# Kernel tuning notes

Measured on AMD Instinct MI355X. Metric: run time of the kernel, lower is better.

## Reference

```python
import jax, jax.numpy as jnp
import numpy as np

# Static config (matches init_kwargs)
H, G, D = 16, 4, 128          # n_head, n_query_groups, head_size
QPK = H // G                  # queries per kv group = 4
LEFT = 1024 - 1               # sliding-window left width (local_window-1)
SCALE = 1.0 / float(np.sqrt(D))
NEG = jnp.finfo(jnp.float32).min


def _rope(x, cos, sin):
    # x: [B,T,h,D]; cos/sin: [T, D/2]; non-interleaved (flash-attn) convention
    d2 = cos.shape[-1]
    x1, x2 = x[..., :d2], x[..., d2:]
    c = cos[None, :, None, :]
    s = sin[None, :, None, :]
    return jnp.concatenate([x1 * c - x2 * s, x1 * s + x2 * c], axis=-1)


def setup_inputs() -> dict:
    key = jax.random.key(0)
    ks = jax.random.split(key, 4)
    B, T, C = 1, 2048, 2048
    x = jax.random.normal(ks[0], (B, T, C), jnp.float32)
    # real RoPE tables, base 10000
    pos = jnp.arange(T, dtype=jnp.float32)
    inv_freq = 1.0 / (10000.0 ** (jnp.arange(0, D, 2, dtype=jnp.float32) / D))
    ang = pos[:, None] * inv_freq[None, :]        # [T, D/2]
    cos, sin = jnp.cos(ang), jnp.sin(ang)
    W_attn = jax.random.normal(ks[1], ((H + 2 * G) * D, C), jnp.float32) * 0.02
    W_proj = jax.random.normal(ks[2], (C, H * D), jnp.float32) * 0.02
    k_sink = jax.random.normal(ks[3], (G * D,), jnp.float32) * 0.02
    v_sink = jnp.zeros((G * D,), jnp.float32)     # buffer, zeros in original
    return {"x": x, "cos": cos, "sin": sin, "W_attn": W_attn,
            "W_proj": W_proj, "k_sink": k_sink, "v_sink": v_sink}


def reference(x, cos, sin, W_attn, W_proj, k_sink, v_sink):
    B, T, C = x.shape
    # fused QKV projection (no bias)
    qkv = jnp.einsum('btc,oc->bto', x, W_attn)                 # [B,T,(H+2G)*D]
    qkv = qkv.reshape(B, T, G, QPK + 2, D)
    q = qkv[:, :, :, :QPK, :].reshape(B, T, H, D)              # [B,T,H,D]
    k = qkv[:, :, :, QPK, :]                                   # [B,T,G,D]
    v = qkv[:, :, :, QPK + 1, :]                               # [B,T,G,D]
    # RoPE on q and k
    q = _rope(q, cos, sin)
    k = _rope(k, cos, sin)
    # prepend sink token to k/v -> seqlen_k = T+1
    k = jnp.concatenate([jnp.broadcast_to(k_sink.reshape(1, 1, G, D), (B, 1, G, D)), k], axis=1)
    v = jnp.concatenate([jnp.broadcast_to(v_sink.reshape(1, 1, G, D), (B, 1, G, D)), v], axis=1)
    Tk = T + 1
    # GQA: group-major query head layout -> head h uses kv group h // QPK
    kh = jnp.repeat(k, QPK, axis=2)                            # [B,Tk,H,D]
    vh = jnp.repeat(v, QPK, axis=2)
    scores = jnp.einsum('bqhd,bkhd->bhqk', q, kh) * SCALE      # [B,H,T,Tk]
    # flash-attn causal + sliding window, bottom-right aligned: offset = Tk - T
    off = Tk - T
    i = jnp.arange(T)[:, None]
    j = jnp.arange(Tk)[None, :]
    allowed = (j <= i + off) & (j >= i + off - LEFT)
    scores = jnp.where(allowed[None, None], scores, NEG)
    p = jax.nn.softmax(scores, axis=-1)
    o = jnp.einsum('bhqk,bkhd->bqhd', p, vh).reshape(B, T, H * D)
    y = jnp.einsum('btd,cd->btc', o, W_proj)                   # output proj, no bias
    return y
```

## Files before the change

### kernel.cpp

```cpp
#include <hip/hip_runtime.h>

#define T_SEQ  2048
#define TK_SEQ 2049
#define JP     2080
#define SL_F    0.12751744f
#define THR_L2  11.0f

typedef __attribute__((ext_vector_type(8))) short short8;
typedef __attribute__((ext_vector_type(4))) float f32x4;

__device__ __forceinline__ unsigned short f2bf(float f) {
  unsigned int u = __float_as_uint(f);
  u += 0x7fff + ((u >> 16) & 1);
  return (unsigned short)(u >> 16);
}

__device__ __forceinline__ void gload16(const unsigned short* g, unsigned short* l) {
  __builtin_amdgcn_global_load_lds(
      (const __attribute__((address_space(1))) void*)g,
      (__attribute__((address_space(3))) void*)l, 16, 0, 0);
}

__global__ __launch_bounds__(256) void split_pack(const float4* __restrict__ s0,
                                                  unsigned short* __restrict__ d0,
                                                  int n0, int p0,
                                                  const float4* __restrict__ s1,
                                                  unsigned short* __restrict__ d1,
                                                  int n1, int p1) {
  int i = blockIdx.x * 256 + threadIdx.x;
  const float4* s; unsigned short* d; int k, p;
  if (i < n0) { s = s0; d = d0; k = i; p = p0; }
  else { k = i - n0; if (k >= n1) return; s = s1; d = d1; p = p1; }
  float4 f = s[k];
  float fv[4] = {f.x, f.y, f.z, f.w};
  ushort4 hv, lv;
#pragma unroll
  for (int e = 0; e < 4; ++e) {
    unsigned int u = __float_as_uint(fv[e]) & 0xffff0000u;
    ((unsigned short*)&hv)[e] = (unsigned short)(u >> 16);
    ((unsigned short*)&lv)[e] = f2bf(fv[e] - __uint_as_float(u));
  }
  *(ushort4*)(d + 4 * (size_t)k)     = hv;
  *(ushort4*)(d + p + 4 * (size_t)k) = lv;
}

__global__ __launch_bounds__(256, 3) void gemm_sp(const unsigned short* __restrict__ Ag,
                                                  const unsigned short* __restrict__ Bg,
                                                  float* __restrict__ C,
                                                  int M, int N, int K) {
  __shared__ unsigned short Ah[128 * 32], Al[128 * 32];
  __shared__ unsigned short Bh[64 * 32],  Bl[64 * 32];

  const int tid  = threadIdx.x;
  const int lane = tid & 63;
  const int wid  = tid >> 6;
  const int wm   = (wid >> 1) << 6;
  const int wn   = (wid & 1) << 5;
  const int lo16 = lane & 15;
  const int hi4  = lane >> 4;
  const int m0   = blockIdx.y << 7;
  const int n0   = blockIdx.x << 6;
  const size_t MK = (size_t)M * K;
  const size_t NK = (size_t)N * K;

  const int ca0 = (wid << 6) + lane;
  const int ca1 = ((4 + wid) << 6) + lane;
  const int cb  = (wid << 6) + lane;
  const unsigned short* a0g = Ag + (size_t)(m0 + (ca0 >> 2)) * K + ((ca0 & 3) << 3);
  const unsigned short* a1g = Ag + (size_t)(m0 + (ca1 >> 2)) * K + ((ca1 & 3) << 3);
  const unsigned short* bg  = Bg + (size_t)(n0 + (cb  >> 2)) * K + ((cb  & 3) << 3);
  unsigned short* a0d  = &Ah[wid << 9];
  unsigned short* a1d  = &Ah[(4 + wid) << 9];
  unsigned short* al0d = &Al[wid << 9];
  unsigned short* al1d = &Al[(4 + wid) << 9];
  unsigned short* bhd  = &Bh[wid << 9];
  unsigned short* bld  = &Bl[wid << 9];

  int ra[4], rb[2];
#pragma unroll
  for (int i = 0; i < 4; ++i) ra[i] = ((wm + i * 16 + lo16) << 5) + (hi4 << 3);
#pragma unroll
  for (int j = 0; j < 2; ++j) rb[j] = ((wn + j * 16 + lo16) << 5) + (hi4 << 3);

  f32x4 acc[4][2];
  const f32x4 z4 = {0.f, 0.f, 0.f, 0.f};
#pragma unroll
  for (int i = 0; i < 4; ++i)
#pragma unroll
    for (int j = 0; j < 2; ++j) acc[i][j] = z4;

  for (int k0 = 0; k0 < K; k0 += 32) {
    __syncthreads();
    gload16(a0g + k0, a0d);
    gload16(a1g + k0, a1d);
    gload16(a0g + MK + k0, al0d);
    gload16(a1g + MK + k0, al1d);
    gload16(bg + k0, bhd);
    gload16(bg + NK + k0, bld);
    __syncthreads();

    short8 fah[4], fal[4], fbh[2], fbl[2];
#pragma unroll
    for (int i = 0; i < 4; ++i) {
      fah[i] = *(const short8*)&Ah[ra[i]];
      fal[i] = *(const short8*)&Al[ra[i]];
    }
#pragma unroll
    for (int j = 0; j < 2; ++j) {
      fbh[j] = *(const short8*)&Bh[rb[j]];
      fbl[j] = *(const short8*)&Bl[rb[j]];
    }
#pragma unroll
    for (int i = 0; i < 4; ++i)
#pragma unroll
      for (int j = 0; j < 2; ++j) {
        acc[i][j] = __builtin_amdgcn_mfma_f32_16x16x32_bf16(fah[i], fbh[j], acc[i][j], 0, 0, 0);
        acc[i][j] = __builtin_amdgcn_mfma_f32_16x16x32_bf16(fal[i], fbh[j], acc[i][j], 0, 0, 0);
        acc[i][j] = __builtin_amdgcn_mfma_f32_16x16x32_bf16(fah[i], fbl[j], acc[i][j], 0, 0, 0);
      }
  }

#pragma unroll
  for (int i = 0; i < 4; ++i) {
    const int row = m0 + wm + i * 16 + (hi4 << 2);
#pragma unroll
    for (int j = 0; j < 2; ++j) {
      float* cp = C + (size_t)row * N + n0 + wn + j * 16 + lo16;
      cp[0]            = acc[i][j][0];
      cp[(size_t)N]    = acc[i][j][1];
      cp[(size_t)2*N]  = acc[i][j][2];
      cp[(size_t)3*N]  = acc[i][j][3];
    }
  }
}

#define RB_Q  4096
#define RB_K  1024
#define RB_KE 64
#define RB_V  65

__global__ __launch_bounds__(256) void rope2(const float* __restrict__ qkv,
                                             const float* __restrict__ cosb,
                                             const float* __restrict__ sinb,
                                             const float* __restrict__ ksink,
                                             const float* __restrict__ vsink,
                                             unsigned short* __restrict__ qb,
                                             unsigned short* __restrict__ kb,
                                             unsigned short* __restrict__ vtb) {
  __shared__ unsigned short tl[512 * 33];
  const int bid = blockIdx.x, tid = threadIdx.x;
  if (bid < RB_Q) {
    int idx = bid * 256 + tid;
    int t = idx >> 9, rem = idx & 511;
    int h = rem >> 5, dp = (rem & 31) << 1;
    int g = h >> 2, qi = h & 3;
    const float* src = qkv + (size_t)t * 3072 + g * 768 + qi * 128;
    float2 x1 = *(const float2*)(src + dp);
    float2 x2 = *(const float2*)(src + 64 + dp);
    float2 c  = *(const float2*)(cosb + t * 64 + dp);
    float2 s  = *(const float2*)(sinb + t * 64 + dp);
    ushort2 o1 = { f2bf(x1.x * c.x - x2.x * s.x), f2bf(x1.y * c.y - x2.y * s.y) };
    ushort2 o2 = { f2bf(x1.x * s.x + x2.x * c.x), f2bf(x1.y * s.y + x2.y * c.y) };
    *(ushort2*)(qb + (size_t)t * 2048 + h * 128 + dp)      = o1;
    *(ushort2*)(qb + (size_t)t * 2048 + h * 128 + 64 + dp) = o2;
  } else if (bid < RB_Q + RB_K) {
    int idx = (bid - RB_Q) * 256 + tid;
    int t = idx >> 7, rem = idx & 127;
    int g = rem >> 5, dp = (rem & 31) << 1;
    const float* src = qkv + (size_t)t * 3072 + g * 768 + 512;
    float2 x1 = *(const float2*)(src + dp);
    float2 x2 = *(const float2*)(src + 64 + dp);
    float2 c  = *(const float2*)(cosb + t * 64 + dp);
    float2 s  = *(const float2*)(sinb + t * 64 + dp);
    ushort2 o1 = { f2bf(x1.x * c.x - x2.x * s.x), f2bf(x1.y * c.y - x2.y * s.y) };
    ushort2 o2 = { f2bf(x1.x * s.x + x2.x * c.x), f2bf(x1.y * s.y + x2.y * c.y) };
    size_t base = (size_t)(t + 1) * 512 + g * 128 + dp;
    *(ushort2*)(kb + base)      = o1;
    *(ushort2*)(kb + base + 64) = o2;
  } else if (bid < RB_Q + RB_K + RB_KE) {
    int idx = (bid - RB_Q - RB_K) * 256 + tid;
    int jj = idx >> 9, c = idx & 511;
    if (jj == 0) kb[c] = f2bf(ksink[c]);
    else         kb[(size_t)(2048 + jj) * 512 + c] = 0;
  } else {
    int b  = bid - RB_Q - RB_K - RB_KE;
    int j0 = b << 5;
#pragma unroll 4
    for (int st = 0; st < 64; ++st) {
      int id = st * 256 + tid;
      int jj = id >> 9, c = id & 511;
      int j = j0 + jj;
      float val;
      if (j == 0)          val = vsink[c];
      else if (j <= T_SEQ) val = qkv[(size_t)(j - 1) * 3072 + (c >> 7) * 768 + 640 + (c & 127)];
      else                 val = 0.f;
      tl[c * 33 + jj] = f2bf(val);
    }
    __syncthreads();
#pragma unroll 4
    for (int st = 0; st < 32; ++st) {
      int id = st * 256 + tid;
      int row = id >> 4, jp = (id & 15) << 1;
      ushort2 w = { tl[row * 33 + jp], tl[row * 33 + jp + 1] };
      *(ushort2*)(vtb + (size_t)row * JP + j0 + jp) = w;
    }
  }
}

#define KSTR 136
#define VSTR 40

__global__ __launch_bounds__(512) void attn_mfma_bf16(const unsigned short* __restrict__ qb,
                                                      const unsigned short* __restrict__ kb,
                                                      const unsigned short* __restrict__ vtb,
                                                      unsigned short* __restrict__ ofh) {
  __shared__ unsigned short Kl[2][32 * KSTR];
  __shared__ unsigned short Vl[2][128 * VSTR];

  const int bid  = blockIdx.x;
  const int tile = bid >> 2;
  const int g    = bid & 3;
  const int t0b  = tile << 5;
  const int tid  = threadIdx.x;
  const int wv   = tid >> 6;
  const int hq   = wv & 3;
  const int sub  = wv >> 2;
  const int h    = g * 4 + hq;
  const int lane = tid & 63;
  const int lo   = lane & 15;
  const int hi   = lane >> 4;
  const int t0w  = t0b + (sub << 4);
  const int t    = t0w + lo;

  const int sj   = tid >> 4;
  const int sc   = (tid & 15) << 3;
  const int kphi = ((((sj & 7) << 2) | (sj >> 3))) * KSTR + sc;
  const int svd  = tid >> 2;
  const int svj  = (tid & 3) << 3;
  const int vdst = svd * VSTR + svj;
  const unsigned short* ksrc = kb  + (size_t)sj * 512 + g * 128 + sc;
  const unsigned short* vsrc = vtb + (size_t)(g * 128 + svd) * JP + svj;

  short8 qfrag[4];
  {
    const unsigned short* qp = qb + (size_t)t * 2048 + h * 128 + (hi << 3);
#pragma unroll
    for (int d0 = 0; d0 < 4; ++d0) qfrag[d0] = *(const short8*)(qp + d0 * 32);
  }

  f32x4 acc[8];
  const f32x4 z4 = {0.f, 0.f, 0.f, 0.f};
#pragma unroll
  for (int dt = 0; dt < 8; ++dt) acc[dt] = z4;

  float m = -1e4f, l = 0.f;

  int jlo = t0b - 1022; if (jlo < 0) jlo = 0;
  const int jb0  = jlo & ~31;
  const int jmax = t0b + 32;
  const int nch  = ((jmax - jb0) >> 5) + 1;

  const int klA = (((lo & 3) << 2) | (lo >> 2)) * KSTR + (hi << 3);

  uint4 kreg = *(const uint4*)(ksrc + (size_t)jb0 * 512);
  uint4 vreg = *(const uint4*)(vsrc + jb0);
  *(uint4*)&Kl[0][kphi] = kreg;
  *(uint4*)&Vl[0][vdst] = vreg;
  __syncthreads();

  int bsel = 0;
  for (int ci = 0; ci < nch; ++ci) {
    const int jb = jb0 + (ci << 5);
    const bool more = (ci + 1 < nch);
    if (more) {
      const int jn = jb + 32;
      kreg = *(const uint4*)(ksrc + (size_t)jn * 512);
      vreg = *(const uint4*)(vsrc + jn);
    }

    const unsigned short* Kb = &Kl[bsel][0];
    f32x4 sa = z4, sb = z4;
#pragma unroll
    for (int d0 = 0; d0 < 4; ++d0) {
      short8 ka  = *(const short8*)(Kb + klA + d0 * 32);
      short8 kB2 = *(const short8*)(Kb + klA + 16 * KSTR + d0 * 32);
      sa = __builtin_amdgcn_mfma_f32_16x16x32_bf16(ka,  qfrag[d0], sa, 0, 0, 0);
      sb = __builtin_amdgcn_mfma_f32_16x16x32_bf16(kB2, qfrag[d0], sb, 0, 0, 0);
    }

    float z[8];
    const int jbase = jb + (hi << 3);
    const bool interior = (jb >= t0w - 1007) && (jb <= t0w - 30);
    if (interior) {
#pragma unroll
      for (int r = 0; r < 4; ++r) { z[r] = sa[r] * SL_F; z[r + 4] = sb[r] * SL_F; }
    } else {
#pragma unroll
      for (int r = 0; r < 8; ++r) {
        float sv = (r < 4) ? sa[r] : sb[r - 4];
        int j = jbase + r;
        bool valid = (j <= t + 1) && (j >= t - 1022);
        z[r] = valid ? sv * SL_F : -1e30f;
      }
    }

    float lmax = fmaxf(fmaxf(fmaxf(z[0], z[1]), fmaxf(z[2], z[3])),
                       fmaxf(fmaxf(z[4], z[5]), fmaxf(z[6], z[7])));
    if (!__all(lmax <= m + THR_L2)) {
      float cm = lmax;
      cm = fmaxf(cm, __shfl_xor(cm, 16, 64));
      cm = fmaxf(cm, __shfl_xor(cm, 32, 64));
      float mn = fmaxf(m, cm);
      float a  = exp2f(m - mn);
      l *= a;
#pragma unroll
      for (int dt = 0; dt < 8; ++dt) acc[dt] *= a;
      m = mn;
    }

    float p[8];
#pragma unroll
    for (int r = 0; r < 8; ++r) { p[r] = exp2f(z[r] - m); l += p[r]; }

    short8 pfrag;
#pragma unroll
    for (int e = 0; e < 8; ++e) pfrag[e] = (short)f2bf(p[e]);

    const unsigned short* Vb = &Vl[bsel][0];
#pragma unroll
    for (int dt = 0; dt < 8; ++dt) {
      short8 vf = *(const short8*)(Vb + (dt * 16 + lo) * VSTR + (hi << 3));
      acc[dt] = __builtin_amdgcn_mfma_f32_16x16x32_bf16(vf, pfrag, acc[dt], 0, 0, 0);
    }

    if (more) {
      *(uint4*)&Kl[bsel ^ 1][kphi] = kreg;
      *(uint4*)&Vl[bsel ^ 1][vdst] = vreg;
      __syncthreads();
      bsel ^= 1;
    }
  }

  float lt = l;
  lt += __shfl_xor(lt, 16, 64);
  lt += __shfl_xor(lt, 32, 64);
  const float inv = 1.f / lt;

  unsigned short* ofl = ofh + 4194304;
  const size_t elem = (size_t)t * 2048 + h * 128 + (hi << 2);
#pragma unroll
  for (int dt = 0; dt < 8; ++dt) {
    f32x4 o4 = acc[dt] * inv;
    ushort4 hv, lv;
#pragma unroll
    for (int e = 0; e < 4; ++e) {
      unsigned int u = __float_as_uint(o4[e]) & 0xffff0000u;
      ((unsigned short*)&hv)[e] = (unsigned short)(u >> 16);
      ((unsigned short*)&lv)[e] = f2bf(o4[e] - __uint_as_float(u));
    }
    *(ushort4*)(ofh + elem + dt * 16) = hv;
    *(ushort4*)(ofl + elem + dt * 16) = lv;
  }
}

extern "C" void kernel_launch(void* const* d_in, const int* in_sizes, int n_in,
                              void* d_out, int out_size, void* d_ws, size_t ws_size,
                              hipStream_t stream) {
  const float* x     = (const float*)d_in[0];
  const float* cosb  = (const float*)d_in[1];
  const float* sinb  = (const float*)d_in[2];
  const float* Wa    = (const float*)d_in[3];
  const float* Wp    = (const float*)d_in[4];
  const float* ksink = (const float*)d_in[5];
  const float* vsink = (const float*)d_in[6];
  float* y = (float*)d_out;

  char* ws = (char*)d_ws;
  float*          qkv = (float*)ws;
  unsigned short* wps = (unsigned short*)ws;
  unsigned short* was = (unsigned short*)(ws + 25165824);
  unsigned short* ofh = (unsigned short*)(ws + 25165824);
  unsigned short* xs  = (unsigned short*)(ws + 50331648);
  unsigned short* qb  = (unsigned short*)(ws + 50331648);
  unsigned short* kbb = (unsigned short*)(ws + 58720256);
  unsigned short* vtb = (unsigned short*)(ws + 60850176);

  split_pack<<<10240, 256, 0, stream>>>((const float4*)x, xs, 1048576, 4194304,
                                        (const float4*)Wa, was, 1572864, 6291456);
  gemm_sp<<<dim3(48, 16), 256, 0, stream>>>(xs, was, qkv, 2048, 3072, 2048);
  rope2<<<RB_Q + RB_K + RB_KE + RB_V, 256, 0, stream>>>(qkv, cosb, sinb, ksink, vsink,
                                                        qb, kbb, vtb);
  split_pack<<<4096, 256, 0, stream>>>((const float4*)Wp, wps, 1048576, 4194304,
                                       (const float4*)Wp, wps, 0, 0);
  attn_mfma_bf16<<<256, 512, 0, stream>>>(qb, kbb, vtb, ofh);
  gemm_sp<<<dim3(32, 16), 256, 0, stream>>>(ofh, wps, y, 2048, 2048, 2048);
}
```

Before: 342.7 us.

## Double-buffer gemm_sp LDS loads and fold W_proj split into attention launch

The split-bf16 GEMM now double-buffers its LDS tiles, issuing the next K-slab's global-to-LDS loads before computing the current one, with explicit vmcnt waits and barriers. This overlaps memory latency with MFMA work at the cost of doubled LDS use, which may cut occupancy under launch_bounds(256,3). Separately, the W_proj hi/lo bf16 split is folded into the attention launch as extra blocks, removing one kernel launch and letting that conversion run alongside the attention blocks.

```diff
diff --git a/kernel.cpp b/kernel.cpp
--- a/kernel.cpp
+++ b/kernel.cpp
@@ -48,8 +48,8 @@
                                                   const unsigned short* __restrict__ Bg,
                                                   float* __restrict__ C,
                                                   int M, int N, int K) {
-  __shared__ unsigned short Ah[128 * 32], Al[128 * 32];
-  __shared__ unsigned short Bh[64 * 32],  Bl[64 * 32];
+  __shared__ unsigned short Ah[2][128 * 32], Al[2][128 * 32];
+  __shared__ unsigned short Bh[2][64 * 32],  Bl[2][64 * 32];
 
   const int tid  = threadIdx.x;
   const int lane = tid & 63;
@@ -65,16 +65,11 @@
 
   const int ca0 = (wid << 6) + lane;
   const int ca1 = ((4 + wid) << 6) + lane;
-  const int cb  = (wid << 6) + lane;
   const unsigned short* a0g = Ag + (size_t)(m0 + (ca0 >> 2)) * K + ((ca0 & 3) << 3);
   const unsigned short* a1g = Ag + (size_t)(m0 + (ca1 >> 2)) * K + ((ca1 & 3) << 3);
-  const unsigned short* bg  = Bg + (size_t)(n0 + (cb  >> 2)) * K + ((cb  & 3) << 3);
-  unsigned short* a0d  = &Ah[wid << 9];
-  unsigned short* a1d  = &Ah[(4 + wid) << 9];
-  unsigned short* al0d = &Al[wid << 9];
-  unsigned short* al1d = &Al[(4 + wid) << 9];
-  unsigned short* bhd  = &Bh[wid << 9];
-  unsigned short* bld  = &Bl[wid << 9];
+  const unsigned short* bg  = Bg + (size_t)(n0 + (ca0 >> 2)) * K + ((ca0 & 3) << 3);
+  const int a0o = wid << 9;
+  const int a1o = (4 + wid) << 9;
 
   int ra[4], rb[2];
 #pragma unroll
@@ -89,26 +84,42 @@
 #pragma unroll
     for (int j = 0; j < 2; ++j) acc[i][j] = z4;
 
+  gload16(a0g,      &Ah[0][a0o]);
+  gload16(a1g,      &Ah[0][a1o]);
+  gload16(a0g + MK, &Al[0][a0o]);
+  gload16(a1g + MK, &Al[0][a1o]);
+  gload16(bg,       &Bh[0][a0o]);
+  gload16(bg + NK,  &Bl[0][a0o]);
+
+  int cur = 0;
   for (int k0 = 0; k0 < K; k0 += 32) {
-    __syncthreads();
-    gload16(a0g + k0, a0d);
-    gload16(a1g + k0, a1d);
-    gload16(a0g + MK + k0, al0d);
-    gload16(a1g + MK + k0, al1d);
-    gload16(bg + k0, bhd);
-    gload16(bg + NK + k0, bld);
-    __syncthreads();
+    const bool more = (k0 + 32) < K;
+    if (more) {
+      const int nxt = cur ^ 1;
+      const int kn  = k0 + 32;
+      gload16(a0g + kn,      &Ah[nxt][a0o]);
+      gload16(a1g + kn,      &Ah[nxt][a1o]);
+      gload16(a0g + MK + kn, &Al[nxt][a0o]);
+      gload16(a1g + MK + kn, &Al[nxt][a1o]);
+      gload16(bg + kn,       &Bh[nxt][a0o]);
+      gload16(bg + NK + kn,  &Bl[nxt][a0o]);
+      asm volatile("s_waitcnt vmcnt(6)" ::: "memory");
+    } else {
+      asm volatile("s_waitcnt vmcnt(0)" ::: "memory");
+    }
+    __builtin_amdgcn_s_barrier();
+    __builtin_amdgcn_sched_barrier(0);
 
     short8 fah[4], fal[4], fbh[2], fbl[2];
 #pragma unroll
     for (int i = 0; i < 4; ++i) {
-      fah[i] = *(const short8*)&Ah[ra[i]];
-      fal[i] = *(const short8*)&Al[ra[i]];
+      fah[i] = *(const short8*)&Ah[cur][ra[i]];
+      fal[i] = *(const short8*)&Al[cur][ra[i]];
     }
 #pragma unroll
     for (int j = 0; j < 2; ++j) {
-      fbh[j] = *(const short8*)&Bh[rb[j]];
-      fbl[j] = *(const short8*)&Bl[rb[j]];
+      fbh[j] = *(const short8*)&Bh[cur][rb[j]];
+      fbl[j] = *(const short8*)&Bl[cur][rb[j]];
     }
 #pragma unroll
     for (int i = 0; i < 4; ++i)
@@ -118,6 +129,11 @@
         acc[i][j] = __builtin_amdgcn_mfma_f32_16x16x32_bf16(fal[i], fbh[j], acc[i][j], 0, 0, 0);
         acc[i][j] = __builtin_amdgcn_mfma_f32_16x16x32_bf16(fah[i], fbl[j], acc[i][j], 0, 0, 0);
       }
+
+    __builtin_amdgcn_sched_barrier(0);
+    __builtin_amdgcn_s_barrier();
+    asm volatile("" ::: "memory");
+    cur ^= 1;
   }
 
 #pragma unroll
@@ -213,15 +229,33 @@
 __global__ __launch_bounds__(512) void attn_mfma_bf16(const unsigned short* __restrict__ qb,
                                                       const unsigned short* __restrict__ kb,
                                                       const unsigned short* __restrict__ vtb,
-                                                      unsigned short* __restrict__ ofh) {
+                                                      unsigned short* __restrict__ ofh,
+                                                      const float4* __restrict__ wpsrc,
+                                                      unsigned short* __restrict__ wps) {
   __shared__ unsigned short Kl[2][32 * KSTR];
   __shared__ unsigned short Vl[2][128 * VSTR];
 
   const int bid  = blockIdx.x;
+  const int tid  = threadIdx.x;
+  if (bid >= 256) {
+    int k = (bid - 256) * 512 + tid;
+    float4 f = wpsrc[k];
+    float fv[4] = {f.x, f.y, f.z, f.w};
+    ushort4 hv, lv;
+#pragma unroll
+    for (int e = 0; e < 4; ++e) {
+      unsigned int u = __float_as_uint(fv[e]) & 0xffff0000u;
+      ((unsigned short*)&hv)[e] = (unsigned short)(u >> 16);
+      ((unsigned short*)&lv)[e] = f2bf(fv[e] - __uint_as_float(u));
+    }
+    *(ushort4*)(wps + 4 * (size_t)k)           = hv;
+    *(ushort4*)(wps + 4194304 + 4 * (size_t)k) = lv;
+    return;
+  }
+
   const int tile = bid >> 2;
   const int g    = bid & 3;
   const int t0b  = tile << 5;
-  const int tid  = threadIdx.x;
   const int wv   = tid >> 6;
   const int hq   = wv & 3;
   const int sub  = wv >> 2;
@@ -390,8 +424,6 @@
   gemm_sp<<<dim3(48, 16), 256, 0, stream>>>(xs, was, qkv, 2048, 3072, 2048);
   rope2<<<RB_Q + RB_K + RB_KE + RB_V, 256, 0, stream>>>(qkv, cosb, sinb, ksink, vsink,
                                                         qb, kbb, vtb);
-  split_pack<<<4096, 256, 0, stream>>>((const float4*)Wp, wps, 1048576, 4194304,
-                                       (const float4*)Wp, wps, 0, 0);
-  attn_mfma_bf16<<<256, 512, 0, stream>>>(qb, kbb, vtb, ofh);
+  attn_mfma_bf16<<<2304, 512, 0, stream>>>(qb, kbb, vtb, ofh, (const float4*)Wp, wps);
   gemm_sp<<<dim3(32, 16), 256, 0, stream>>>(ofh, wps, y, 2048, 2048, 2048);
 }
```

Result: no change. 342.1 us (-0.2%).
